# Optimization experiments

Measured on AMD Instinct MI355X. Metric: run time of the kernel, lower is better.

The kernel has to match this reference:

```python
import math
import jax, jax.numpy as jnp
import numpy as np

N_HEAD = 16
ROPE_BASE = 10000.0


def _rope_tables(T, half, dtype):
    # build_sin_cos(seq_len, dim=head_dim//2): inv freq of length `half`
    pos = jnp.arange(T, dtype=jnp.float32)[:, None]                       # (T,1)
    inv = jnp.exp(jnp.arange(0, 2 * half, 2, dtype=jnp.float32) * (-math.log(ROPE_BASE) / (2 * half)))
    ang = pos * inv                                                        # (T, half)
    return jnp.sin(ang).astype(dtype), jnp.cos(ang).astype(dtype)


def _apply_rope(q, k, sin, cos):
    # q,k: (B,T,H,Dh); sin,cos: (T, Dh//2) -> broadcast over batch and heads
    half = q.shape[-1] // 2
    s = sin[None, :, None, :]
    c = cos[None, :, None, :]
    q1, q2 = q[..., :half], q[..., half:]
    k1, k2 = k[..., :half], k[..., half:]
    q = jnp.concatenate([q1 * c - q2 * s, q2 * c + q1 * s], axis=-1)
    k = jnp.concatenate([k1 * c - k2 * s, k2 * c + k1 * s], axis=-1)
    return q, k


def setup_inputs() -> dict:
    key = jax.random.key(0)
    k1, k2, k3 = jax.random.split(key, 3)
    B, T, C = 2, 2048, 2048
    x = jax.random.normal(k1, (B, T, C), dtype=jnp.float32)
    w_qkv = jax.random.normal(k2, (3 * C, C), dtype=jnp.float32) * (1.0 / math.sqrt(C))
    w_proj = jax.random.normal(k3, (C, C), dtype=jnp.float32) * (1.0 / math.sqrt(C))
    return {"x": x, "w_qkv": w_qkv, "w_proj": w_proj}


def reference(x, w_qkv, w_proj):
    B, T, C = x.shape
    H = N_HEAD
    Dh = C // H
    # fused QKV projection (Linear, no bias): (B,T,3C) -> (B,T,3,H,Dh)
    qkv = jnp.einsum('btc,oc->bto', x, w_qkv).reshape(B, T, 3, H, Dh)
    q, k, v = qkv[:, :, 0], qkv[:, :, 1], qkv[:, :, 2]          # (B,T,H,Dh)
    sin, cos = _rope_tables(T, Dh // 2, x.dtype)
    q, k = _apply_rope(q, k, sin, cos)
    # causal attention, scale 1/sqrt(Dh) (flash default softmax_scale=None)
    scale = 1.0 / math.sqrt(Dh)
    scores = jnp.einsum('bqhd,bkhd->bhqk', q, k) * scale        # (B,H,T,T)
    mask = jnp.tril(jnp.ones((T, T), dtype=bool))
    scores = jnp.where(mask[None, None], scores, jnp.finfo(scores.dtype).min)
    probs = jax.nn.softmax(scores, axis=-1)
    out = jnp.einsum('bhqk,bkhd->bqhd', probs, v)               # (B,T,H,Dh)
    # faithful to original: permute(0,2,1,3) then reshape_as(x)
    out = jnp.transpose(out, (0, 2, 1, 3)).reshape(B, T, C)
    return jnp.einsum('btc,oc->bto', out, w_proj)
```

## Files before the change

kernel.cpp:

```cpp
#include <hip/hip_runtime.h>
#include <hip/hip_bf16.h>

typedef __bf16 bf16_t;
typedef __bf16 bf16x8 __attribute__((ext_vector_type(8)));
typedef float f32x4 __attribute__((ext_vector_type(4)));

#define MFMA16(a, b, c) __builtin_amdgcn_mfma_f32_16x16x32_bf16(a, b, c, 0, 0, 0)

__device__ __forceinline__ void async_copy16(const void* g, void* l) {
  __builtin_amdgcn_global_load_lds(
      (const __attribute__((address_space(1))) void*)g,
      (__attribute__((address_space(3))) void*)l, 16, 0, 0);
}

__global__ void cast_f32_bf16(const float* __restrict__ in, bf16_t* __restrict__ out, int n8) {
  int stride = gridDim.x * blockDim.x;
  for (int i = blockIdx.x * blockDim.x + threadIdx.x; i < n8; i += stride) {
    const float* p = in + (size_t)i * 8;
    f32x4 a = *(const f32x4*)p;
    f32x4 b = *(const f32x4*)(p + 4);
    bf16x8 o;
    o[0] = (bf16_t)a[0]; o[1] = (bf16_t)a[1]; o[2] = (bf16_t)a[2]; o[3] = (bf16_t)a[3];
    o[4] = (bf16_t)b[0]; o[5] = (bf16_t)b[1]; o[6] = (bf16_t)b[2]; o[7] = (bf16_t)b[3];
    *(bf16x8*)(out + (size_t)i * 8) = o;
  }
}

template <int MODE>
__global__ __launch_bounds__(256) void gemm_bt(
    const bf16_t* __restrict__ A, const bf16_t* __restrict__ Bw, float* __restrict__ C,
    bf16_t* __restrict__ qo, bf16_t* __restrict__ ko, bf16_t* __restrict__ vto,
    int M, int N, int K) {
  __shared__ bf16_t lds[2][2][128 * 32];
  int tid = threadIdx.x;
  int w = tid >> 6, lane = tid & 63;
  int wm = w >> 1, wn = w & 1;
  int mr = lane & 15, kg = lane >> 4;
  int row0 = blockIdx.y * 128;
  int col0 = blockIdx.x * 128;

  auto stage = [&](int buf, int t) {
#pragma unroll
    for (int it = 0; it < 2; ++it) {
      int chunk = it * 256 + tid;
      int r = chunk >> 2, cb = (chunk & 3) * 8;
      async_copy16(A + (size_t)(row0 + r) * K + t * 32 + cb, &lds[buf][0][chunk * 8]);
    }
#pragma unroll
    for (int it = 0; it < 2; ++it) {
      int chunk = it * 256 + tid;
      int r = chunk >> 2, cb = (chunk & 3) * 8;
      async_copy16(Bw + (size_t)(col0 + r) * K + t * 32 + cb, &lds[buf][1][chunk * 8]);
    }
  };

  f32x4 zero = {0.f, 0.f, 0.f, 0.f};
  f32x4 acc[4][4];
#pragma unroll
  for (int i = 0; i < 4; ++i)
#pragma unroll
    for (int jn = 0; jn < 4; ++jn) acc[i][jn] = zero;

  int nt = K / 32, cur = 0;
  stage(0, 0);
  for (int t = 0; t < nt; ++t) {
    __syncthreads();
    if (t + 1 < nt) stage(cur ^ 1, t + 1);
    const bf16_t* As = &lds[cur][0][0];
    const bf16_t* Bs = &lds[cur][1][0];
    bf16x8 af[4], bfr[4];
#pragma unroll
    for (int i = 0; i < 4; ++i)
      af[i] = *(const bf16x8*)(As + (wm * 64 + i * 16 + mr) * 32 + kg * 8);
#pragma unroll
    for (int i = 0; i < 4; ++i)
      bfr[i] = *(const bf16x8*)(Bs + (wn * 64 + i * 16 + mr) * 32 + kg * 8);
#pragma unroll
    for (int i = 0; i < 4; ++i)
#pragma unroll
      for (int jn = 0; jn < 4; ++jn)
        acc[i][jn] = MFMA16(af[i], bfr[jn], acc[i][jn]);
    cur ^= 1;
  }

  if (MODE == 0) {
#pragma unroll
    for (int i = 0; i < 4; ++i)
#pragma unroll
      for (int jn = 0; jn < 4; ++jn)
#pragma unroll
        for (int jj = 0; jj < 4; ++jj) {
          int row = row0 + wm * 64 + i * 16 + kg * 4 + jj;
          int col = col0 + wn * 64 + jn * 16 + mr;
          C[(size_t)row * N + col] = acc[i][jn][jj];
        }
  } else {
    __syncthreads();
    char* tb = (char*)&lds[0][0][0];
    int s = col0 >> 11, h = (col0 >> 7) & 15;
    int b = row0 >> 11, t0 = row0 & 2047;
    if (s < 2) {
#pragma unroll
      for (int i = 0; i < 4; ++i)
#pragma unroll
        for (int jn = 0; jn < 4; ++jn)
#pragma unroll
          for (int jj = 0; jj < 4; ++jj) {
            int row = wm * 64 + i * 16 + kg * 4 + jj;
            int col = wn * 64 + jn * 16 + mr;
            *(bf16_t*)(tb + row * 256 + ((col * 2) ^ ((row & 7) << 4))) =
                (bf16_t)acc[i][jn][jj];
          }
      __syncthreads();
      int r = tid >> 1, hh = tid & 1;
      int t = t0 + r;
      const char* rowb = tb + r * 256;
      int sz = (r & 7) << 4;
      bf16_t* dst = (s == 0 ? qo : ko) +
                    ((size_t)((b * 16 + h) * 2048 + t)) * 128 + hh * 64;
      float tf = (float)t;
      const float cinv = -0.20762050593046014f;
#pragma unroll
      for (int m = 0; m < 8; ++m) {
        bf16x8 va = *(const bf16x8*)(rowb + ((hh * 128 + m * 16) ^ sz));
        bf16x8 vb = *(const bf16x8*)(rowb + (((hh ^ 1) * 128 + m * 16) ^ sz));
        bf16x8 o;
#pragma unroll
        for (int e = 0; e < 8; ++e) {
          float ang = tf * exp2f((float)(m * 8 + e) * cinv);
          float sv = __sinf(ang), cv = __cosf(ang);
          float x1 = (float)va[e], x2 = (float)vb[e];
          float res = (hh == 0) ? (x1 * cv - x2 * sv) : (x1 * cv + x2 * sv);
          o[e] = (bf16_t)res;
        }
        *(bf16x8*)(dst + m * 8) = o;
      }
    } else {
#pragma unroll
      for (int i = 0; i < 4; ++i)
#pragma unroll
        for (int jn = 0; jn < 4; ++jn)
#pragma unroll
          for (int jj = 0; jj < 4; ++jj) {
            int row = wm * 64 + i * 16 + kg * 4 + jj;
            int col = wn * 64 + jn * 16 + mr;
            *(bf16_t*)(tb + col * 256 + ((row * 2) ^ ((col & 7) << 4))) =
                (bf16_t)acc[i][jn][jj];
          }
      __syncthreads();
      int d = tid >> 1, tseg = (tid & 1) * 64;
      const char* rowb = tb + d * 256;
      int sz = (d & 7) << 4;
      bf16_t* dst = vto + ((size_t)((b * 16 + h) * 128 + d)) * 2048 + t0 + tseg;
#pragma unroll
      for (int m2 = 0; m2 < 8; ++m2)
        *(bf16x8*)(dst + m2 * 8) = *(const bf16x8*)(rowb + ((tseg * 2 + m2 * 16) ^ sz));
    }
  }
}

__global__ __launch_bounds__(256) void attn_kernel(
    const bf16_t* __restrict__ qg, const bf16_t* __restrict__ kgl,
    const bf16_t* __restrict__ vtg, bf16_t* __restrict__ og) {
  __shared__ __align__(16) bf16_t Ks[2][64 * 128];
  __shared__ __align__(16) bf16_t Vs[2][128 * 64];
  __shared__ __align__(16) bf16_t plds[4][1024];
  const int T = 2048;
  int tid = threadIdx.x;
  int w = tid >> 6, lane = tid & 63;
  int mr = lane & 15, kg = lane >> 4;
  int swz = (mr & 7) << 4;

  int L = blockIdx.y * 16 + blockIdx.x;
  int role = (L & 7) * 64 + (L >> 3);
  int bx = role & 15, bh = role >> 4;

  const bf16_t* Q = qg + (size_t)bh * T * 128;
  const bf16_t* K = kgl + (size_t)bh * T * 128;
  const bf16_t* Vt = vtg + (size_t)bh * 128 * T;

  int sb = tid * 16;
  int krl = sb >> 8;
  int kc = (sb & 255) ^ ((krl & 7) << 4);
  size_t ksrc = (size_t)krl * 128 + (kc >> 1);
  int vdl = sb >> 7;
  int vc = (sb & 127) ^ ((vdl & 7) << 4);
  size_t vsrc = (size_t)vdl * 2048 + (vc >> 1);

  auto stage = [&](int buf, int kb) {
#pragma unroll
    for (int it = 0; it < 4; ++it)
      async_copy16(K + (size_t)(kb + it * 16) * 128 + ksrc, &Ks[buf][it * 2048 + tid * 8]);
#pragma unroll
    for (int it = 0; it < 4; ++it)
      async_copy16(Vt + (size_t)it * 65536 + kb + vsrc, &Vs[buf][it * 2048 + tid * 8]);
  };

  const float cscale = 0.12751744f;
  f32x4 zero = {0.f, 0.f, 0.f, 0.f};
  bf16_t* P = &plds[w][0];
  int b = bh >> 4, h = bh & 15;

#pragma unroll 1
  for (int ph = 0; ph < 2; ++ph) {
    int qb = ph ? bx : (31 - bx);
    int qr0 = qb * 64 + w * 16;
    bf16x8 qf[4];
#pragma unroll
    for (int db = 0; db < 4; ++db)
      qf[db] = *(const bf16x8*)(Q + (size_t)(qr0 + mr) * 128 + db * 32 + kg * 8);

    f32x4 acc[8];
#pragma unroll
    for (int d2 = 0; d2 < 8; ++d2) acc[d2] = zero;
    float mrun[4] = {-1e30f, -1e30f, -1e30f, -1e30f};
    float lrun[4] = {0.f, 0.f, 0.f, 0.f};

    int nj = qb + 1;
    __syncthreads();
    stage(0, 0);
    int cur = 0;
#pragma unroll 1
    for (int j = 0; j < nj; ++j) {
      __syncthreads();
      if (j + 1 < nj) stage(cur ^ 1, (j + 1) * 64);
      const char* KsB = (const char*)&Ks[cur][0];
      const char* VsB = (const char*)&Vs[cur][0];
      int kb = j * 64;
      f32x4 s[4];
#pragma unroll
      for (int ntl = 0; ntl < 4; ++ntl) {
        s[ntl] = zero;
        int rowb = (ntl * 16 + mr) * 256;
#pragma unroll
        for (int db = 0; db < 4; ++db) {
          bf16x8 kf = *(const bf16x8*)(KsB + rowb + ((db * 64 + kg * 16) ^ swz));
          s[ntl] = MFMA16(qf[db], kf, s[ntl]);
        }
      }
      float pvv[4][4];
      float tmax[4] = {-3e38f, -3e38f, -3e38f, -3e38f};
      bool diag = (j == qb);
#pragma unroll
      for (int ntl = 0; ntl < 4; ++ntl)
#pragma unroll
        for (int jj = 0; jj < 4; ++jj) {
          float v = s[ntl][jj] * cscale;
          if (diag && (kb + ntl * 16 + mr) > (qr0 + kg * 4 + jj)) v = -1e30f;
          pvv[ntl][jj] = v;
          tmax[jj] = fmaxf(tmax[jj], v);
        }
#pragma unroll
      for (int m = 1; m < 16; m <<= 1)
#pragma unroll
        for (int jj = 0; jj < 4; ++jj)
          tmax[jj] = fmaxf(tmax[jj], __shfl_xor(tmax[jj], m, 64));
      bool ok = true;
#pragma unroll
      for (int jj = 0; jj < 4; ++jj) ok &= (tmax[jj] <= mrun[jj] + 8.0f);
      if (!__all(ok)) {
#pragma unroll
        for (int jj = 0; jj < 4; ++jj) {
          float mn = fmaxf(mrun[jj], tmax[jj]);
          float corr = __builtin_amdgcn_exp2f(mrun[jj] - mn);
          mrun[jj] = mn;
          lrun[jj] *= corr;
#pragma unroll
          for (int d2 = 0; d2 < 8; ++d2) acc[d2][jj] *= corr;
        }
      }
      float rs[4] = {0.f, 0.f, 0.f, 0.f};
#pragma unroll
      for (int ntl = 0; ntl < 4; ++ntl)
#pragma unroll
        for (int jj = 0; jj < 4; ++jj) {
          float p = __builtin_amdgcn_exp2f(pvv[ntl][jj] - mrun[jj]);
          pvv[ntl][jj] = p;
          rs[jj] += p;
        }
#pragma unroll
      for (int m = 1; m < 16; m <<= 1)
#pragma unroll
        for (int jj = 0; jj < 4; ++jj) rs[jj] += __shfl_xor(rs[jj], m, 64);
#pragma unroll
      for (int jj = 0; jj < 4; ++jj) lrun[jj] += rs[jj];
#pragma unroll
      for (int ntl = 0; ntl < 4; ++ntl)
#pragma unroll
        for (int jj = 0; jj < 4; ++jj) {
          int rr = kg * 4 + jj;
          int cbyte = (mr + ntl * 16) * 2;
          *(bf16_t*)((char*)P + rr * 128 + (cbyte ^ ((rr & 7) << 4))) = (bf16_t)pvv[ntl][jj];
        }
#pragma unroll
      for (int ks = 0; ks < 2; ++ks) {
        int cb = (ks * 32 + kg * 8) * 2;
        bf16x8 pa = *(const bf16x8*)((const char*)P + mr * 128 + (cb ^ ((mr & 7) << 4)));
#pragma unroll
        for (int d2 = 0; d2 < 8; ++d2) {
          bf16x8 vf = *(const bf16x8*)(VsB + (d2 * 16 + mr) * 128 + ((ks * 64 + kg * 16) ^ swz));
          acc[d2] = MFMA16(pa, vf, acc[d2]);
        }
      }
      cur ^= 1;
    }
#pragma unroll
    for (int jj = 0; jj < 4; ++jj) {
      float invl = 1.0f / lrun[jj];
      int t = qr0 + kg * 4 + jj;
      size_t row = (size_t)b * 2048 + h * 128 + (t >> 4);
      bf16_t* orow = og + row * 2048 + (t & 15) * 128;
#pragma unroll
      for (int d2 = 0; d2 < 8; ++d2)
        orow[d2 * 16 + mr] = (bf16_t)(acc[d2][jj] * invl);
    }
  }
}

extern "C" void kernel_launch(void* const* d_in, const int* in_sizes, int n_in,
                              void* d_out, int out_size, void* d_ws, size_t ws_size,
                              hipStream_t stream) {
  const float* x = (const float*)d_in[0];
  const float* wqkv = (const float*)d_in[1];
  const float* wproj = (const float*)d_in[2];
  float* out = (float*)d_out;
  char* ws = (char*)d_ws;

  const size_t OFF_WQKV = 16777216;
  const size_t OFF_Q = 41943040;
  const size_t OFF_K = 58720256;
  const size_t OFF_VT = 75497472;

  bf16_t* xb = (bf16_t*)(ws);
  bf16_t* wqkvb = (bf16_t*)(ws + OFF_WQKV);
  bf16_t* g_q = (bf16_t*)(ws + OFF_Q);
  bf16_t* g_k = (bf16_t*)(ws + OFF_K);
  bf16_t* g_vt = (bf16_t*)(ws + OFF_VT);
  bf16_t* g_att = (bf16_t*)(ws);
  bf16_t* wprojb = (bf16_t*)(ws + OFF_WQKV);

  cast_f32_bf16<<<2048, 256, 0, stream>>>(x, xb, 8388608 / 8);
  cast_f32_bf16<<<2048, 256, 0, stream>>>(wqkv, wqkvb, 12582912 / 8);
  gemm_bt<1><<<dim3(48, 32), 256, 0, stream>>>(xb, wqkvb, nullptr, g_q, g_k, g_vt,
                                               4096, 6144, 2048);
  cast_f32_bf16<<<2048, 256, 0, stream>>>(wproj, wprojb, 4194304 / 8);
  attn_kernel<<<dim3(16, 32), 256, 0, stream>>>(g_q, g_k, g_vt, g_att);
  gemm_bt<0><<<dim3(16, 32), 256, 0, stream>>>(g_att, wprojb, out, nullptr, nullptr,
                                               nullptr, 4096, 2048, 2048);
}
```

Baseline: 281.5 us.

## Rewrite GEMM as 256x128 tile, 512-thread kernel with swizzled LDS and XCD remap

```diff
diff --git a/kernel.cpp b/kernel.cpp
--- a/kernel.cpp
+++ b/kernel.cpp
@@ -27,97 +27,131 @@
 }
 
 template <int MODE>
-__global__ __launch_bounds__(256) void gemm_bt(
+__global__ __launch_bounds__(512, 2) void gemm256(
     const bf16_t* __restrict__ A, const bf16_t* __restrict__ Bw, float* __restrict__ C,
     bf16_t* __restrict__ qo, bf16_t* __restrict__ ko, bf16_t* __restrict__ vto,
-    int M, int N, int K) {
-  __shared__ bf16_t lds[2][2][128 * 32];
+    int M, int N, int K, int nby) {
+  __shared__ __align__(16) char lds[98304];
   int tid = threadIdx.x;
   int w = tid >> 6, lane = tid & 63;
   int wm = w >> 1, wn = w & 1;
   int mr = lane & 15, kg = lane >> 4;
-  int row0 = blockIdx.y * 128;
-  int col0 = blockIdx.x * 128;
-
-  auto stage = [&](int buf, int t) {
-#pragma unroll
-    for (int it = 0; it < 2; ++it) {
-      int chunk = it * 256 + tid;
-      int r = chunk >> 2, cb = (chunk & 3) * 8;
-      async_copy16(A + (size_t)(row0 + r) * K + t * 32 + cb, &lds[buf][0][chunk * 8]);
-    }
-#pragma unroll
-    for (int it = 0; it < 2; ++it) {
-      int chunk = it * 256 + tid;
-      int r = chunk >> 2, cb = (chunk & 3) * 8;
-      async_copy16(Bw + (size_t)(col0 + r) * K + t * 32 + cb, &lds[buf][1][chunk * 8]);
-    }
+
+  int nwg = gridDim.x;
+  int orig = blockIdx.x;
+  int wgid = (orig & 7) * (nwg >> 3) + (orig >> 3);
+  int by = wgid % nby, bx = wgid / nby;
+  int row0 = by * 256, col0 = bx * 128;
+
+  size_t aoff[4], boff[2];
+#pragma unroll
+  for (int it = 0; it < 4; ++it) {
+    int c = tid + it * 512;
+    int r = c >> 3;
+    int chs = (c & 7) ^ (r & 7);
+    aoff[it] = (size_t)(row0 + r) * K + chs * 8;
+  }
+#pragma unroll
+  for (int it = 0; it < 2; ++it) {
+    int c = tid + it * 512;
+    int r = c >> 3;
+    int chs = (c & 7) ^ (r & 7);
+    boff[it] = (size_t)(col0 + r) * K + chs * 8;
+  }
+
+  auto stage = [&](int buf, int kt) {
+    char* Ad = &lds[buf * 32768];
+    char* Bd = &lds[65536 + buf * 16384];
+#pragma unroll
+    for (int it = 0; it < 4; ++it)
+      async_copy16(A + aoff[it] + kt * 64, Ad + (tid + it * 512) * 16);
+#pragma unroll
+    for (int it = 0; it < 2; ++it)
+      async_copy16(Bw + boff[it] + kt * 64, Bd + (tid + it * 512) * 16);
   };
 
   f32x4 zero = {0.f, 0.f, 0.f, 0.f};
   f32x4 acc[4][4];
 #pragma unroll
-  for (int i = 0; i < 4; ++i)
-#pragma unroll
-    for (int jn = 0; jn < 4; ++jn) acc[i][jn] = zero;
-
-  int nt = K / 32, cur = 0;
+  for (int mi = 0; mi < 4; ++mi)
+#pragma unroll
+    for (int ni = 0; ni < 4; ++ni) acc[mi][ni] = zero;
+
+  int nt = K >> 6;
   stage(0, 0);
+#pragma unroll 1
   for (int t = 0; t < nt; ++t) {
-    __syncthreads();
-    if (t + 1 < nt) stage(cur ^ 1, t + 1);
-    const bf16_t* As = &lds[cur][0][0];
-    const bf16_t* Bs = &lds[cur][1][0];
-    bf16x8 af[4], bfr[4];
-#pragma unroll
-    for (int i = 0; i < 4; ++i)
-      af[i] = *(const bf16x8*)(As + (wm * 64 + i * 16 + mr) * 32 + kg * 8);
-#pragma unroll
-    for (int i = 0; i < 4; ++i)
-      bfr[i] = *(const bf16x8*)(Bs + (wn * 64 + i * 16 + mr) * 32 + kg * 8);
-#pragma unroll
-    for (int i = 0; i < 4; ++i)
-#pragma unroll
-      for (int jn = 0; jn < 4; ++jn)
-        acc[i][jn] = MFMA16(af[i], bfr[jn], acc[i][jn]);
-    cur ^= 1;
-  }
+    int cur = t & 1;
+    stage(cur ^ 1, (t + 1 < nt) ? (t + 1) : t);
+    asm volatile("s_waitcnt vmcnt(6)" ::: "memory");
+    __builtin_amdgcn_sched_barrier(0);
+    __builtin_amdgcn_s_barrier();
+    __builtin_amdgcn_sched_barrier(0);
+    const char* Ab = &lds[cur * 32768];
+    const char* Bb = &lds[65536 + cur * 16384];
+    bf16x8 af[4][2];
+#pragma unroll
+    for (int mi = 0; mi < 4; ++mi) {
+      int row = wm * 64 + mi * 16 + mr;
+      const char* rb = Ab + row * 128;
+      int sz = (row & 7) << 4;
+      af[mi][0] = *(const bf16x8*)(rb + ((kg * 16) ^ sz));
+      af[mi][1] = *(const bf16x8*)(rb + ((64 + kg * 16) ^ sz));
+    }
+#pragma unroll
+    for (int ni = 0; ni < 4; ++ni) {
+      int row = wn * 64 + ni * 16 + mr;
+      const char* rb = Bb + row * 128;
+      int sz = (row & 7) << 4;
+      bf16x8 b0 = *(const bf16x8*)(rb + ((kg * 16) ^ sz));
+      bf16x8 b1 = *(const bf16x8*)(rb + ((64 + kg * 16) ^ sz));
+      __builtin_amdgcn_s_setprio(1);
+#pragma unroll
+      for (int mi = 0; mi < 4; ++mi) {
+        acc[mi][ni] = MFMA16(af[mi][0], b0, acc[mi][ni]);
+        acc[mi][ni] = MFMA16(af[mi][1], b1, acc[mi][ni]);
+      }
+      __builtin_amdgcn_s_setprio(0);
+    }
+    __builtin_amdgcn_sched_barrier(0);
+    __builtin_amdgcn_s_barrier();
+    __builtin_amdgcn_sched_barrier(0);
+  }
+  asm volatile("s_waitcnt vmcnt(0)" ::: "memory");
+  __syncthreads();
 
   if (MODE == 0) {
 #pragma unroll
-    for (int i = 0; i < 4; ++i)
-#pragma unroll
-      for (int jn = 0; jn < 4; ++jn)
-#pragma unroll
-        for (int jj = 0; jj < 4; ++jj) {
-          int row = row0 + wm * 64 + i * 16 + kg * 4 + jj;
-          int col = col0 + wn * 64 + jn * 16 + mr;
-          C[(size_t)row * N + col] = acc[i][jn][jj];
+    for (int mi = 0; mi < 4; ++mi)
+#pragma unroll
+      for (int ni = 0; ni < 4; ++ni)
+#pragma unroll
+        for (int jj = 0; jj < 4; ++jj) {
+          int row = row0 + wm * 64 + mi * 16 + kg * 4 + jj;
+          int col = col0 + wn * 64 + ni * 16 + mr;
+          C[(size_t)row * N + col] = acc[mi][ni][jj];
         }
   } else {
-    __syncthreads();
-    char* tb = (char*)&lds[0][0][0];
+    char* tb = &lds[0];
     int s = col0 >> 11, h = (col0 >> 7) & 15;
     int b = row0 >> 11, t0 = row0 & 2047;
     if (s < 2) {
 #pragma unroll
-      for (int i = 0; i < 4; ++i)
-#pragma unroll
-        for (int jn = 0; jn < 4; ++jn)
+      for (int mi = 0; mi < 4; ++mi)
+#pragma unroll
+        for (int ni = 0; ni < 4; ++ni)
 #pragma unroll
           for (int jj = 0; jj < 4; ++jj) {
-            int row = wm * 64 + i * 16 + kg * 4 + jj;
-            int col = wn * 64 + jn * 16 + mr;
-            *(bf16_t*)(tb + row * 256 + ((col * 2) ^ ((row & 7) << 4))) =
-                (bf16_t)acc[i][jn][jj];
+            int rloc = wm * 64 + mi * 16 + kg * 4 + jj;
+            int cb = (wn * 64 + ni * 16 + mr) * 2;
+            *(bf16_t*)(tb + rloc * 256 + (cb ^ ((rloc & 7) << 4))) = (bf16_t)acc[mi][ni][jj];
           }
       __syncthreads();
       int r = tid >> 1, hh = tid & 1;
-      int t = t0 + r;
       const char* rowb = tb + r * 256;
       int sz = (r & 7) << 4;
-      bf16_t* dst = (s == 0 ? qo : ko) +
-                    ((size_t)((b * 16 + h) * 2048 + t)) * 128 + hh * 64;
+      int t = t0 + r;
+      bf16_t* dst = (s == 0 ? qo : ko) + ((size_t)((b * 16 + h) * 2048 + t)) * 128 + hh * 64;
       float tf = (float)t;
       const float cinv = -0.20762050593046014f;
 #pragma unroll
@@ -130,31 +164,30 @@
           float ang = tf * exp2f((float)(m * 8 + e) * cinv);
           float sv = __sinf(ang), cv = __cosf(ang);
           float x1 = (float)va[e], x2 = (float)vb[e];
-          float res = (hh == 0) ? (x1 * cv - x2 * sv) : (x1 * cv + x2 * sv);
-          o[e] = (bf16_t)res;
+          o[e] = (bf16_t)((hh == 0) ? (x1 * cv - x2 * sv) : (x1 * cv + x2 * sv));
         }
         *(bf16x8*)(dst + m * 8) = o;
       }
     } else {
 #pragma unroll
-      for (int i = 0; i < 4; ++i)
-#pragma unroll
-        for (int jn = 0; jn < 4; ++jn)
+      for (int mi = 0; mi < 4; ++mi)
+#pragma unroll
+        for (int ni = 0; ni < 4; ++ni)
 #pragma unroll
           for (int jj = 0; jj < 4; ++jj) {
-            int row = wm * 64 + i * 16 + kg * 4 + jj;
-            int col = wn * 64 + jn * 16 + mr;
-            *(bf16_t*)(tb + col * 256 + ((row * 2) ^ ((col & 7) << 4))) =
-                (bf16_t)acc[i][jn][jj];
+            int rloc = wm * 64 + mi * 16 + kg * 4 + jj;
+            int cloc = wn * 64 + ni * 16 + mr;
+            *(bf16_t*)(tb + cloc * 512 + ((rloc * 2) ^ ((cloc & 7) << 4))) =
+                (bf16_t)acc[mi][ni][jj];
           }
       __syncthreads();
-      int d = tid >> 1, tseg = (tid & 1) * 64;
-      const char* rowb = tb + d * 256;
+      int d = tid >> 2, qt = tid & 3;
+      const char* rowb = tb + d * 512;
       int sz = (d & 7) << 4;
-      bf16_t* dst = vto + ((size_t)((b * 16 + h) * 128 + d)) * 2048 + t0 + tseg;
+      bf16_t* dst = vto + ((size_t)((b * 16 + h) * 128 + d)) * 2048 + t0 + qt * 64;
 #pragma unroll
       for (int m2 = 0; m2 < 8; ++m2)
-        *(bf16x8*)(dst + m2 * 8) = *(const bf16x8*)(rowb + ((tseg * 2 + m2 * 16) ^ sz));
+        *(bf16x8*)(dst + m2 * 8) = *(const bf16x8*)(rowb + ((qt * 128 + m2 * 16) ^ sz));
     }
   }
 }
@@ -341,10 +374,10 @@
 
   cast_f32_bf16<<<2048, 256, 0, stream>>>(x, xb, 8388608 / 8);
   cast_f32_bf16<<<2048, 256, 0, stream>>>(wqkv, wqkvb, 12582912 / 8);
-  gemm_bt<1><<<dim3(48, 32), 256, 0, stream>>>(xb, wqkvb, nullptr, g_q, g_k, g_vt,
-                                               4096, 6144, 2048);
+  gemm256<1><<<768, 512, 0, stream>>>(xb, wqkvb, nullptr, g_q, g_k, g_vt,
+                                      4096, 6144, 2048, 16);
   cast_f32_bf16<<<2048, 256, 0, stream>>>(wproj, wprojb, 4194304 / 8);
   attn_kernel<<<dim3(16, 32), 256, 0, stream>>>(g_q, g_k, g_vt, g_att);
-  gemm_bt<0><<<dim3(16, 32), 256, 0, stream>>>(g_att, wprojb, out, nullptr, nullptr,
-                                               nullptr, 4096, 2048, 2048);
-}
+  gemm256<0><<<256, 512, 0, stream>>>(g_att, wprojb, out, nullptr, nullptr, nullptr,
+                                      4096, 2048, 2048, 16);
+}
```

Measured after the change: 286.1 us. Within noise of the previous version (+1.6%).
